# Kernel optimization log

Measured on AMD Instinct MI355X. Metric: run time of the kernel, lower is better.

The kernel has to match this reference:

```python
import jax, jax.numpy as jnp
import numpy as np

EMB = 768
B, LD, LW, LH = 2, 8, 8, 8        # LR grid = number of windows per axis
HD, HW, HH = 32, 32, 32           # HR volume
LN_EPS = 1e-5


def setup_inputs() -> dict:
    key = jax.random.key(0)
    ks = jax.random.split(key, 12)
    s = 1.0 / np.sqrt(EMB)
    inp = {
        "LR_image": jax.random.normal(ks[0], (B, LD, LW, LH, EMB), jnp.float32),
        "HR_image": jax.random.normal(ks[1], (B, HD, HW, HH, EMB), jnp.float32),
        "Wq_w": jax.random.uniform(ks[2], (EMB, EMB), jnp.float32, -s, s),
        "Wq_b": jax.random.uniform(ks[3], (EMB,), jnp.float32, -s, s),
        "Wk_w": jax.random.uniform(ks[4], (EMB, EMB), jnp.float32, -s, s),
        "Wk_b": jax.random.uniform(ks[5], (EMB,), jnp.float32, -s, s),
        "Wv_w": jax.random.uniform(ks[6], (EMB, EMB), jnp.float32, -s, s),
        "Wv_b": jax.random.uniform(ks[7], (EMB,), jnp.float32, -s, s),
        "Wo_w": jax.random.uniform(ks[8], (EMB, EMB), jnp.float32, -s, s),
        "Wo_b": jax.random.uniform(ks[9], (EMB,), jnp.float32, -s, s),
        "ln_g": jnp.ones((EMB,), jnp.float32),
        "ln_b": jnp.zeros((EMB,), jnp.float32),
        "S_d": 4, "S_w": 4, "S_h": 4,
    }
    return inp


def _window_partition(x, S_d, S_w, S_h):
    # x: [B, D, W, H, C] -> [B, N_blocks, S_d*S_w*S_h, C]
    b, d, w, h, c = x.shape
    x = x.reshape(b, d // S_d, S_d, w // S_w, S_w, h // S_h, S_h, c)
    x = jnp.transpose(x, (0, 2, 4, 6, 1, 3, 5, 7))  # [B,Sd,Sw,Sh,Db,Wb,Hb,C]
    x = x.reshape(b, S_d * S_w * S_h, -1, c)
    return jnp.transpose(x, (0, 2, 1, 3))  # [B, N_blocks, S, C]


def reference(LR_image, HR_image, Wq_w, Wq_b, Wk_w, Wk_b, Wv_w, Wv_b,
              Wo_w, Wo_b, ln_g, ln_b, S_d, S_w, S_h):
    b = LR_image.shape[0]
    c = LR_image.shape[-1]
    # queries: [B, N, 1, C]
    q_in = LR_image.reshape(b, -1, c)[:, :, None, :]
    # windowed keys/values: [B, N, S, C]
    hr = _window_partition(HR_image, S_d, S_w, S_h)
    q = q_in @ Wq_w.T + Wq_b
    k = hr @ Wk_w.T + Wk_b
    v = hr @ Wv_w.T + Wv_b
    scale = 1.0 / jnp.sqrt(jnp.asarray(c, q.dtype))
    scores = jnp.einsum('bnqc,bnsc->bnqs', q, k) * scale  # [B,N,1,S]
    attn = jax.nn.softmax(scores, axis=-1)
    x = jnp.einsum('bnqs,bnsc->bnqc', attn, v).reshape(b, -1, c)
    x = x @ Wo_w.T + Wo_b
    res = q.reshape(b, -1, c) + x  # residual with projected queries
    mu = jnp.mean(res, axis=-1, keepdims=True)
    var = jnp.var(res, axis=-1, keepdims=True)
    return (res - mu) / jnp.sqrt(var + LN_EPS) * ln_g + ln_b
```

## Files before the change

### kernel.cpp

```cpp
#include <hip/hip_runtime.h>
#include <hip/hip_bf16.h>
#include <math.h>

#define EMB 768
#define NB 2
#define NWIN 512
#define NROWS (NB*NWIN)
#define SWIN 64
#define HRDIM 32
#define ROWF (NROWS*EMB)
#define WELEM (EMB*EMB)

using bfrag = __attribute__((ext_vector_type(8))) short;
using f32x4 = __attribute__((ext_vector_type(4))) float;

#define GL16(g, l)  __builtin_amdgcn_global_load_lds(                         \
    (const __attribute__((address_space(1))) void*)(g),                       \
    (__attribute__((address_space(3))) void*)(l), 16, 0, 0)

__global__ __launch_bounds__(256)
void prep_kernel(const float* __restrict__ LR, __hip_bfloat16* __restrict__ LRb,
                 const float* __restrict__ Wq, __hip_bfloat16* __restrict__ Wqb,
                 const float* __restrict__ Wo, __hip_bfloat16* __restrict__ Wob,
                 __hip_bfloat16* __restrict__ WqTb,
                 const float* __restrict__ Wk, __hip_bfloat16* __restrict__ WkTb,
                 const float* __restrict__ Wv, __hip_bfloat16* __restrict__ WvTb,
                 const float* __restrict__ bq, const float* __restrict__ bv,
                 const float* __restrict__ bo,
                 float* __restrict__ bqk, float* __restrict__ bvo) {
  __shared__ float tile[32][33];
  const int bx = blockIdx.x;
  const int t = threadIdx.x;

  if (bx < 960) {
    const float* in; __hip_bfloat16* out; int i;
    if (bx < 384)      { in = LR; out = LRb; i = bx * 256 + t; }
    else if (bx < 672) { in = Wq; out = Wqb; i = (bx - 384) * 256 + t; }
    else               { in = Wo; out = Wob; i = (bx - 672) * 256 + t; }
    float4 a = *(const float4*)&in[(size_t)i * 8];
    float4 b = *(const float4*)&in[(size_t)i * 8 + 4];
    __hip_bfloat16 o[8];
    o[0] = __float2bfloat16(a.x); o[1] = __float2bfloat16(a.y);
    o[2] = __float2bfloat16(a.z); o[3] = __float2bfloat16(a.w);
    o[4] = __float2bfloat16(b.x); o[5] = __float2bfloat16(b.y);
    o[6] = __float2bfloat16(b.z); o[7] = __float2bfloat16(b.w);
    *(uint4*)&out[(size_t)i * 8] = *(const uint4*)o;
  } else if (bx < 2688) {
    int idx = bx - 960;
    int z = idx / 576, rem = idx % 576;
    int bi = rem % 24, bj = rem / 24;
    const float* in; __hip_bfloat16* out;
    if (z == 0)      { in = Wq; out = WqTb; }
    else if (z == 1) { in = Wk; out = WkTb; }
    else             { in = Wv; out = WvTb; }
    const int c = t & 31, r8 = t >> 5;
#pragma unroll
    for (int rr = 0; rr < 4; ++rr) {
      int r = r8 + rr * 8;
      tile[c][r] = in[(size_t)(bi * 32 + r) * EMB + bj * 32 + c];
    }
    __syncthreads();
#pragma unroll
    for (int rr = 0; rr < 4; ++rr) {
      int n = r8 + rr * 8;
      out[(size_t)(bj * 32 + n) * EMB + bi * 32 + c] = __float2bfloat16(tile[n][c]);
    }
  } else {
    int idx = bx - 2688;
    if (idx < 12) {
      __shared__ float red[4][64];
      const int io = t & 63, cg = t >> 6;
      const int i = idx * 64 + io;
      float s = 0.f;
#pragma unroll 8
      for (int c = cg; c < EMB; c += 4)
        s = fmaf(bq[c], Wk[(size_t)c * EMB + i], s);
      red[cg][io] = s;
      __syncthreads();
      if (cg == 0)
        bqk[i] = red[0][io] + red[1][io] + red[2][io] + red[3][io];
    } else {
      const int w = t >> 6, lane = t & 63;
      const int p = (idx - 12) * 4 + w;
      float s = 0.f;
#pragma unroll
      for (int r = 0; r < 12; ++r) {
        int n = lane + r * 64;
        s = fmaf(Wo[(size_t)p * EMB + n], bv[n], s);
      }
#pragma unroll
      for (int o = 32; o > 0; o >>= 1) s += __shfl_xor(s, o, 64);
      if (lane == 0) bvo[p] = bo[p] + s;
    }
  }
}

template<bool BIAS, bool WF32, bool WB16, bool RESID>
__global__ __launch_bounds__(256)
void gemm128(const __hip_bfloat16* __restrict__ A0,
             const __hip_bfloat16* __restrict__ A1,
             const __hip_bfloat16* __restrict__ B0,
             const __hip_bfloat16* __restrict__ B1,
             const float* __restrict__ bias0, const float* __restrict__ bias1,
             float* __restrict__ Cf0, float* __restrict__ Cf1,
             __hip_bfloat16* __restrict__ Cb0, __hip_bfloat16* __restrict__ Cb1,
             const float* __restrict__ R0, const float* __restrict__ R1,
             int N) {
  constexpr int K = EMB;
  constexpr int NT = K / 64;
  const int zi = blockIdx.z;
  const __hip_bfloat16* A  = zi ? A1 : A0;
  const __hip_bfloat16* Bm = zi ? B1 : B0;
  const float* bias = zi ? bias1 : bias0;
  float* Cf = zi ? Cf1 : Cf0;
  __hip_bfloat16* Cb = zi ? Cb1 : Cb0;
  const float* R = zi ? R1 : R0;

  __shared__ short lsA[3][128 * 64];
  __shared__ short lsB[3][128 * 64];
  const int t = threadIdx.x;
  const int w = t >> 6, lane = t & 63;
  const int lr = lane & 15, lk = lane >> 4;
  const int wr = w >> 1, wc = w & 1;
  const int m0 = blockIdx.y * 128, n0 = blockIdx.x * 128;

  const int r0 = t >> 3;
  const int kc = (t & 7) ^ (r0 & 7);
  const __hip_bfloat16* aptr = A + (size_t)(m0 + r0) * K + kc * 8;
  const __hip_bfloat16* bptr = Bm + (size_t)(n0 + r0) * K + kc * 8;
  const int wb512 = w * 512;

#define STAGE128(sl, ko)                                                      \
  do {                                                                        \
    GL16(aptr + 0 * 32 * K + (ko), &lsA[sl][0 * 2048 + wb512]);               \
    GL16(aptr + 1 * 32 * K + (ko), &lsA[sl][1 * 2048 + wb512]);               \
    GL16(aptr + 2 * 32 * K + (ko), &lsA[sl][2 * 2048 + wb512]);               \
    GL16(aptr + 3 * 32 * K + (ko), &lsA[sl][3 * 2048 + wb512]);               \
    GL16(bptr + 0 * 32 * K + (ko), &lsB[sl][0 * 2048 + wb512]);               \
    GL16(bptr + 1 * 32 * K + (ko), &lsB[sl][1 * 2048 + wb512]);               \
    GL16(bptr + 2 * 32 * K + (ko), &lsB[sl][2 * 2048 + wb512]);               \
    GL16(bptr + 3 * 32 * K + (ko), &lsB[sl][3 * 2048 + wb512]);               \
  } while (0)

  int aoff[4][2], boff[4][2];
#pragma unroll
  for (int f = 0; f < 4; ++f) {
    int ar = wr * 64 + f * 16 + lr;
    int br = wc * 64 + f * 16 + lr;
#pragma unroll
    for (int ks = 0; ks < 2; ++ks) {
      aoff[f][ks] = ar * 64 + ((((ks << 2) | lk) ^ (ar & 7)) << 3);
      boff[f][ks] = br * 64 + ((((ks << 2) | lk) ^ (br & 7)) << 3);
    }
  }

  f32x4 acc[4][4];
#pragma unroll
  for (int i = 0; i < 4; ++i)
#pragma unroll
    for (int j = 0; j < 4; ++j) acc[i][j] = (f32x4){0.f, 0.f, 0.f, 0.f};

  STAGE128(0, 0);
  STAGE128(1, 64);

#pragma unroll
  for (int kt = 0; kt < NT; ++kt) {
    if (kt + 2 < NT) {
      constexpr int s3[NT + 2] = {0,1,2,0,1,2,0,1,2,0,1,2,0,1};
      STAGE128(s3[kt + 2], (kt + 2) * 64);
    }
    if (kt + 2 < NT)      asm volatile("s_waitcnt vmcnt(16)" ::: "memory");
    else if (kt + 1 < NT) asm volatile("s_waitcnt vmcnt(8)" ::: "memory");
    else                  asm volatile("s_waitcnt vmcnt(0)" ::: "memory");
    __builtin_amdgcn_sched_barrier(0);
    __builtin_amdgcn_s_barrier();

    const int cur = kt % 3;
#pragma unroll
    for (int ks = 0; ks < 2; ++ks) {
      bfrag a_[4], b_[4];
#pragma unroll
      for (int f = 0; f < 4; ++f) {
        a_[f] = *(const bfrag*)&lsA[cur][aoff[f][ks]];
        b_[f] = *(const bfrag*)&lsB[cur][boff[f][ks]];
      }
#pragma unroll
      for (int i = 0; i < 4; ++i)
#pragma unroll
        for (int j = 0; j < 4; ++j)
          acc[i][j] = __builtin_amdgcn_mfma_f32_16x16x32_bf16(
              a_[i], b_[j], acc[i][j], 0, 0, 0);
    }

    asm volatile("s_waitcnt lgkmcnt(0)" ::: "memory");
    __builtin_amdgcn_s_barrier();
    __builtin_amdgcn_sched_barrier(0);
  }
#undef STAGE128

  float bs[4];
#pragma unroll
  for (int j = 0; j < 4; ++j)
    bs[j] = BIAS ? bias[n0 + wc * 64 + j * 16 + lr] : 0.f;

#pragma unroll
  for (int i = 0; i < 4; ++i) {
#pragma unroll
    for (int j = 0; j < 4; ++j) {
      int n = n0 + wc * 64 + j * 16 + lr;
#pragma unroll
      for (int q = 0; q < 4; ++q) {
        int m = m0 + wr * 64 + i * 16 + lk * 4 + q;
        float v = acc[i][j][q] + bs[j];
        if (RESID) v += R[(size_t)m * N + n];
        if (WF32) Cf[(size_t)m * N + n] = v;
        if (WB16) Cb[(size_t)m * N + n] = __float2bfloat16(v);
      }
    }
  }
}

__global__ __launch_bounds__(512)
void attn_kernel(const float* __restrict__ HR, const float* __restrict__ qt,
                 __hip_bfloat16* __restrict__ zb) {
  const int g = blockIdx.x;
  const int b = g >> 9;
  const int n = g & 511;
  const int db = n >> 6, wb = (n >> 3) & 7, hb = n & 7;

  __shared__ float zp[8][EMB];
  __shared__ float ml[8][2];

  const int t = threadIdx.x;
  const int w = t >> 6, lane = t & 63;

  float4 qv[3];
#pragma unroll
  for (int r = 0; r < 3; ++r)
    qv[r] = *(const float4*)&qt[(size_t)g * EMB + (lane + r * 64) * 4];

  const float* rows[8];
#pragma unroll
  for (int i = 0; i < 8; ++i) {
    int s = w * 8 + i;
    int D = db * 4 + (s >> 4), W = wb * 4 + ((s >> 2) & 3), H = hb * 4 + (s & 3);
    rows[i] = HR + (size_t)((((b * HRDIM + D) * HRDIM + W) * HRDIM + H)) * EMB;
  }

  const float scale = 0.036084391824351615f;
  float m = -3.0e38f, l = 0.f;
  float4 z0 = {0,0,0,0}, z1 = {0,0,0,0}, z2 = {0,0,0,0};

  float4 h0 = *(const float4*)&rows[0][lane * 4];
  float4 h1 = *(const float4*)&rows[0][(lane + 64) * 4];
  float4 h2 = *(const float4*)&rows[0][(lane + 128) * 4];

#pragma unroll
  for (int i = 0; i < 8; ++i) {
    float4 n0, n1, n2;
    if (i < 7) {
      n0 = *(const float4*)&rows[i + 1][lane * 4];
      n1 = *(const float4*)&rows[i + 1][(lane + 64) * 4];
      n2 = *(const float4*)&rows[i + 1][(lane + 128) * 4];
    }
    float p = 0.f;
    p = fmaf(h0.x, qv[0].x, p); p = fmaf(h0.y, qv[0].y, p);
    p = fmaf(h0.z, qv[0].z, p); p = fmaf(h0.w, qv[0].w, p);
    p = fmaf(h1.x, qv[1].x, p); p = fmaf(h1.y, qv[1].y, p);
    p = fmaf(h1.z, qv[1].z, p); p = fmaf(h1.w, qv[1].w, p);
    p = fmaf(h2.x, qv[2].x, p); p = fmaf(h2.y, qv[2].y, p);
    p = fmaf(h2.z, qv[2].z, p); p = fmaf(h2.w, qv[2].w, p);
#pragma unroll
    for (int o = 32; o > 0; o >>= 1) p += __shfl_xor(p, o, 64);
    p *= scale;
    float mn = fmaxf(m, p);
    float f = expf(m - mn);
    float e = expf(p - mn);
    z0.x = fmaf(e, h0.x, z0.x * f); z0.y = fmaf(e, h0.y, z0.y * f);
    z0.z = fmaf(e, h0.z, z0.z * f); z0.w = fmaf(e, h0.w, z0.w * f);
    z1.x = fmaf(e, h1.x, z1.x * f); z1.y = fmaf(e, h1.y, z1.y * f);
    z1.z = fmaf(e, h1.z, z1.z * f); z1.w = fmaf(e, h1.w, z1.w * f);
    z2.x = fmaf(e, h2.x, z2.x * f); z2.y = fmaf(e, h2.y, z2.y * f);
    z2.z = fmaf(e, h2.z, z2.z * f); z2.w = fmaf(e, h2.w, z2.w * f);
    l = fmaf(l, f, e);
    m = mn;
    if (i < 7) { h0 = n0; h1 = n1; h2 = n2; }
  }

  *(float4*)&zp[w][lane * 4] = z0;
  *(float4*)&zp[w][(lane + 64) * 4] = z1;
  *(float4*)&zp[w][(lane + 128) * 4] = z2;
  if (lane == 0) { ml[w][0] = m; ml[w][1] = l; }
  __syncthreads();

  if (t < 384) {
    float M = -3.0e38f;
#pragma unroll
    for (int w8 = 0; w8 < 8; ++w8) M = fmaxf(M, ml[w8][0]);
    float L = 0.f, a0 = 0.f, a1 = 0.f;
#pragma unroll
    for (int w8 = 0; w8 < 8; ++w8) {
      float ew = expf(ml[w8][0] - M);
      L = fmaf(ml[w8][1], ew, L);
      float2 v = *(const float2*)&zp[w8][t * 2];
      a0 = fmaf(v.x, ew, a0);
      a1 = fmaf(v.y, ew, a1);
    }
    float rl = 1.f / L;
    __hip_bfloat16 o[2];
    o[0] = __float2bfloat16(a0 * rl);
    o[1] = __float2bfloat16(a1 * rl);
    *(unsigned*)&zb[(size_t)g * EMB + t * 2] = *(const unsigned*)o;
  }
}

__global__ __launch_bounds__(256)
void ln_kernel(const float* __restrict__ R, const float* __restrict__ gma,
               const float* __restrict__ bta, float* __restrict__ out) {
  const int row = blockIdx.x;
  const int t = threadIdx.x;
  const int wave = t >> 6, lane = t & 63;
  __shared__ float red[4];

  float v[3];
  float s = 0.f;
#pragma unroll
  for (int r = 0; r < 3; ++r) {
    int c = t + r * 256;
    v[r] = R[(size_t)row * EMB + c];
    s += v[r];
  }
#pragma unroll
  for (int o = 32; o > 0; o >>= 1) s += __shfl_xor(s, o, 64);
  if (lane == 0) red[wave] = s;
  __syncthreads();
  float mu = (red[0] + red[1] + red[2] + red[3]) * (1.f / EMB);
  __syncthreads();

  float q = 0.f;
#pragma unroll
  for (int r = 0; r < 3; ++r) {
    float d = v[r] - mu;
    q += d * d;
  }
#pragma unroll
  for (int o = 32; o > 0; o >>= 1) q += __shfl_xor(q, o, 64);
  if (lane == 0) red[wave] = q;
  __syncthreads();
  float var = (red[0] + red[1] + red[2] + red[3]) * (1.f / EMB);
  float inv = rsqrtf(var + 1e-5f);

#pragma unroll
  for (int r = 0; r < 3; ++r) {
    int c = t + r * 256;
    out[(size_t)row * EMB + c] = (v[r] - mu) * inv * gma[c] + bta[c];
  }
}

extern "C" void kernel_launch(void* const* d_in, const int* in_sizes, int n_in,
                              void* d_out, int out_size, void* d_ws, size_t ws_size,
                              hipStream_t stream) {
  const float* LR  = (const float*)d_in[0];
  const float* HR  = (const float*)d_in[1];
  const float* Wq  = (const float*)d_in[2];
  const float* bq  = (const float*)d_in[3];
  const float* Wk  = (const float*)d_in[4];
  const float* Wv  = (const float*)d_in[6];
  const float* bv  = (const float*)d_in[7];
  const float* Wo  = (const float*)d_in[8];
  const float* bo  = (const float*)d_in[9];
  const float* lng = (const float*)d_in[10];
  const float* lnb = (const float*)d_in[11];
  float* out = (float*)d_out;

  char* ws = (char*)d_ws;
  float* Qf = (float*)(ws + 0);
  float* qt = (float*)(ws + 3145728);
  float* x  = (float*)(ws + 6291456);
  __hip_bfloat16* LRb  = (__hip_bfloat16*)(ws +  9437184);
  __hip_bfloat16* zb   = (__hip_bfloat16*)(ws + 11010048);
  __hip_bfloat16* Wqb  = (__hip_bfloat16*)(ws + 12582912);
  __hip_bfloat16* Wob  = (__hip_bfloat16*)(ws + 13762560);
  __hip_bfloat16* WqTb = (__hip_bfloat16*)(ws + 14942208);
  __hip_bfloat16* WkTb = (__hip_bfloat16*)(ws + 16121856);
  __hip_bfloat16* WvTb = (__hip_bfloat16*)(ws + 17301504);
  __hip_bfloat16* Wqkb = (__hip_bfloat16*)(ws + 18481152);
  __hip_bfloat16* Wvob = (__hip_bfloat16*)(ws + 19660800);
  float* bqk = (float*)(ws + 20840448);
  float* bvo = (float*)(ws + 20843520);

  dim3 blk(256);

  prep_kernel<<<dim3(2892), blk, 0, stream>>>(
      LR, LRb, Wq, Wqb, Wo, Wob, WqTb, Wk, WkTb, Wv, WvTb,
      bq, bv, bo, bqk, bvo);
  gemm128<false, false, true, false><<<dim3(6, 6, 2), blk, 0, stream>>>(
      WkTb, Wob, WqTb, WvTb, nullptr, nullptr,
      nullptr, nullptr, Wqkb, Wvob, nullptr, nullptr, EMB);
  gemm128<true, true, false, false><<<dim3(6, 8, 2), blk, 0, stream>>>(
      LRb, LRb, Wqb, Wqkb, bq, bqk, Qf, qt, nullptr, nullptr,
      nullptr, nullptr, EMB);
  attn_kernel<<<dim3(NROWS), dim3(512), 0, stream>>>(HR, qt, zb);
  gemm128<true, true, false, true><<<dim3(6, 8, 1), blk, 0, stream>>>(
      zb, zb, Wvob, Wvob, bvo, bvo, x, x, nullptr, nullptr, Qf, Qf, EMB);
  ln_kernel<<<dim3(NROWS), blk, 0, stream>>>(x, lng, lnb, out);
}
```

Before: 87.52 us.

## Compute qt from projected Q instead of folded Wq·Wk; merge GEMMs with atomic dependency

Drops the precomputed Wq^T·Wk weight product and the bq·Wk bias. The key-folded query qt is now computed as Q_bf16 @ Wk, which picks up the query bias implicitly, so one weight-weight GEMM and the WqT transpose go away. The Q projection, the Wv·Wo fold and the qt GEMM are merged into a single three-slice launch. The qt slice spin-waits on a global atomic counter that the 48 Q tiles increment, which removes kernel launches. The risks are deadlock if the z=2 blocks are scheduled before the z=0 blocks and fill the GPU (bounded by an iteration cap), and the GEMM templates becoming runtime branches.

```diff
diff --git a/kernel.cpp b/kernel.cpp
--- a/kernel.cpp
+++ b/kernel.cpp
@@ -22,12 +22,10 @@
 void prep_kernel(const float* __restrict__ LR, __hip_bfloat16* __restrict__ LRb,
                  const float* __restrict__ Wq, __hip_bfloat16* __restrict__ Wqb,
                  const float* __restrict__ Wo, __hip_bfloat16* __restrict__ Wob,
-                 __hip_bfloat16* __restrict__ WqTb,
                  const float* __restrict__ Wk, __hip_bfloat16* __restrict__ WkTb,
                  const float* __restrict__ Wv, __hip_bfloat16* __restrict__ WvTb,
-                 const float* __restrict__ bq, const float* __restrict__ bv,
-                 const float* __restrict__ bo,
-                 float* __restrict__ bqk, float* __restrict__ bvo) {
+                 const float* __restrict__ bv, const float* __restrict__ bo,
+                 float* __restrict__ bvo, int* __restrict__ ctr) {
   __shared__ float tile[32][33];
   const int bx = blockIdx.x;
   const int t = threadIdx.x;
@@ -45,14 +43,13 @@
     o[4] = __float2bfloat16(b.x); o[5] = __float2bfloat16(b.y);
     o[6] = __float2bfloat16(b.z); o[7] = __float2bfloat16(b.w);
     *(uint4*)&out[(size_t)i * 8] = *(const uint4*)o;
-  } else if (bx < 2688) {
+  } else if (bx < 2112) {
     int idx = bx - 960;
     int z = idx / 576, rem = idx % 576;
     int bi = rem % 24, bj = rem / 24;
     const float* in; __hip_bfloat16* out;
-    if (z == 0)      { in = Wq; out = WqTb; }
-    else if (z == 1) { in = Wk; out = WkTb; }
-    else             { in = Wv; out = WvTb; }
+    if (z == 0) { in = Wk; out = WkTb; }
+    else        { in = Wv; out = WvTb; }
     const int c = t & 31, r8 = t >> 5;
 #pragma unroll
     for (int rr = 0; rr < 4; ++rr) {
@@ -66,55 +63,60 @@
       out[(size_t)(bj * 32 + n) * EMB + bi * 32 + c] = __float2bfloat16(tile[n][c]);
     }
   } else {
-    int idx = bx - 2688;
-    if (idx < 12) {
-      __shared__ float red[4][64];
-      const int io = t & 63, cg = t >> 6;
-      const int i = idx * 64 + io;
-      float s = 0.f;
-#pragma unroll 8
-      for (int c = cg; c < EMB; c += 4)
-        s = fmaf(bq[c], Wk[(size_t)c * EMB + i], s);
-      red[cg][io] = s;
-      __syncthreads();
-      if (cg == 0)
-        bqk[i] = red[0][io] + red[1][io] + red[2][io] + red[3][io];
-    } else {
-      const int w = t >> 6, lane = t & 63;
-      const int p = (idx - 12) * 4 + w;
-      float s = 0.f;
-#pragma unroll
-      for (int r = 0; r < 12; ++r) {
-        int n = lane + r * 64;
-        s = fmaf(Wo[(size_t)p * EMB + n], bv[n], s);
-      }
-#pragma unroll
-      for (int o = 32; o > 0; o >>= 1) s += __shfl_xor(s, o, 64);
-      if (lane == 0) bvo[p] = bo[p] + s;
-    }
+    int idx = bx - 2112;
+    if (idx == 0 && t == 0) *ctr = 0;
+    const int w = t >> 6, lane = t & 63;
+    const int p = idx * 4 + w;
+    float s = 0.f;
+#pragma unroll
+    for (int r = 0; r < 12; ++r) {
+      int n = lane + r * 64;
+      s = fmaf(Wo[(size_t)p * EMB + n], bv[n], s);
+    }
+#pragma unroll
+    for (int o = 32; o > 0; o >>= 1) s += __shfl_xor(s, o, 64);
+    if (lane == 0) bvo[p] = bo[p] + s;
   }
 }
 
-template<bool BIAS, bool WF32, bool WB16, bool RESID>
 __global__ __launch_bounds__(256)
 void gemm128(const __hip_bfloat16* __restrict__ A0,
+             const __hip_bfloat16* __restrict__ B0,
+             const float* __restrict__ bias0, float* __restrict__ Cf0,
+             __hip_bfloat16* __restrict__ Cb0, const float* __restrict__ R0,
              const __hip_bfloat16* __restrict__ A1,
-             const __hip_bfloat16* __restrict__ B0,
              const __hip_bfloat16* __restrict__ B1,
-             const float* __restrict__ bias0, const float* __restrict__ bias1,
-             float* __restrict__ Cf0, float* __restrict__ Cf1,
-             __hip_bfloat16* __restrict__ Cb0, __hip_bfloat16* __restrict__ Cb1,
-             const float* __restrict__ R0, const float* __restrict__ R1,
-             int N) {
+             const float* __restrict__ bias1, float* __restrict__ Cf1,
+             __hip_bfloat16* __restrict__ Cb1,
+             const __hip_bfloat16* __restrict__ A2,
+             const __hip_bfloat16* __restrict__ B2,
+             const float* __restrict__ bias2, float* __restrict__ Cf2,
+             __hip_bfloat16* __restrict__ Cb2,
+             int* ctr, int N, int ylim1) {
   constexpr int K = EMB;
   constexpr int NT = K / 64;
   const int zi = blockIdx.z;
-  const __hip_bfloat16* A  = zi ? A1 : A0;
-  const __hip_bfloat16* Bm = zi ? B1 : B0;
-  const float* bias = zi ? bias1 : bias0;
-  float* Cf = zi ? Cf1 : Cf0;
-  __hip_bfloat16* Cb = zi ? Cb1 : Cb0;
-  const float* R = zi ? R1 : R0;
+  const __hip_bfloat16* A  = (zi == 0) ? A0 : (zi == 1) ? A1 : A2;
+  const __hip_bfloat16* Bm = (zi == 0) ? B0 : (zi == 1) ? B1 : B2;
+  const float* bias = (zi == 0) ? bias0 : (zi == 1) ? bias1 : bias2;
+  float* Cf = (zi == 0) ? Cf0 : (zi == 1) ? Cf1 : Cf2;
+  __hip_bfloat16* Cb = (zi == 0) ? Cb0 : (zi == 1) ? Cb1 : Cb2;
+  const float* R = (zi == 0) ? R0 : nullptr;
+
+  if (zi == 1 && (int)blockIdx.y >= ylim1) return;
+
+  if (ctr && zi == 2) {
+    if ((threadIdx.x & 63) == 0) {
+      int it = 0;
+      while (__hip_atomic_load(ctr, __ATOMIC_ACQUIRE,
+                               __HIP_MEMORY_SCOPE_AGENT) < 48 &&
+             it < (1 << 20)) {
+        __builtin_amdgcn_s_sleep(4);
+        ++it;
+      }
+    }
+    __syncthreads();
+  }
 
   __shared__ short lsA[3][128 * 64];
   __shared__ short lsB[3][128 * 64];
@@ -201,7 +203,7 @@
   float bs[4];
 #pragma unroll
   for (int j = 0; j < 4; ++j)
-    bs[j] = BIAS ? bias[n0 + wc * 64 + j * 16 + lr] : 0.f;
+    bs[j] = bias ? bias[n0 + wc * 64 + j * 16 + lr] : 0.f;
 
 #pragma unroll
   for (int i = 0; i < 4; ++i) {
@@ -212,11 +214,19 @@
       for (int q = 0; q < 4; ++q) {
         int m = m0 + wr * 64 + i * 16 + lk * 4 + q;
         float v = acc[i][j][q] + bs[j];
-        if (RESID) v += R[(size_t)m * N + n];
-        if (WF32) Cf[(size_t)m * N + n] = v;
-        if (WB16) Cb[(size_t)m * N + n] = __float2bfloat16(v);
+        if (R) v += R[(size_t)m * N + n];
+        if (Cf) Cf[(size_t)m * N + n] = v;
+        if (Cb) Cb[(size_t)m * N + n] = __float2bfloat16(v);
       }
     }
+  }
+
+  if (ctr && zi == 0) {
+    __threadfence();
+    __syncthreads();
+    if (threadIdx.x == 0)
+      __hip_atomic_fetch_add(ctr, 1, __ATOMIC_RELEASE,
+                             __HIP_MEMORY_SCOPE_AGENT);
   }
 }
 
@@ -379,29 +389,33 @@
   float* x  = (float*)(ws + 6291456);
   __hip_bfloat16* LRb  = (__hip_bfloat16*)(ws +  9437184);
   __hip_bfloat16* zb   = (__hip_bfloat16*)(ws + 11010048);
-  __hip_bfloat16* Wqb  = (__hip_bfloat16*)(ws + 12582912);
-  __hip_bfloat16* Wob  = (__hip_bfloat16*)(ws + 13762560);
-  __hip_bfloat16* WqTb = (__hip_bfloat16*)(ws + 14942208);
-  __hip_bfloat16* WkTb = (__hip_bfloat16*)(ws + 16121856);
-  __hip_bfloat16* WvTb = (__hip_bfloat16*)(ws + 17301504);
-  __hip_bfloat16* Wqkb = (__hip_bfloat16*)(ws + 18481152);
-  __hip_bfloat16* Wvob = (__hip_bfloat16*)(ws + 19660800);
-  float* bqk = (float*)(ws + 20840448);
-  float* bvo = (float*)(ws + 20843520);
+  __hip_bfloat16* Qbb  = (__hip_bfloat16*)(ws + 12582912);
+  __hip_bfloat16* Wqb  = (__hip_bfloat16*)(ws + 14155776);
+  __hip_bfloat16* WkTb = (__hip_bfloat16*)(ws + 15335424);
+  __hip_bfloat16* WvTb = (__hip_bfloat16*)(ws + 16515072);
+  __hip_bfloat16* Wob  = (__hip_bfloat16*)(ws + 17694720);
+  __hip_bfloat16* Wvob = (__hip_bfloat16*)(ws + 18874368);
+  float* bvo = (float*)(ws + 20054016);
+  int*   ctr = (int*)(ws + 20971520);
 
   dim3 blk(256);
 
-  prep_kernel<<<dim3(2892), blk, 0, stream>>>(
-      LR, LRb, Wq, Wqb, Wo, Wob, WqTb, Wk, WkTb, Wv, WvTb,
-      bq, bv, bo, bqk, bvo);
-  gemm128<false, false, true, false><<<dim3(6, 6, 2), blk, 0, stream>>>(
-      WkTb, Wob, WqTb, WvTb, nullptr, nullptr,
-      nullptr, nullptr, Wqkb, Wvob, nullptr, nullptr, EMB);
-  gemm128<true, true, false, false><<<dim3(6, 8, 2), blk, 0, stream>>>(
-      LRb, LRb, Wqb, Wqkb, bq, bqk, Qf, qt, nullptr, nullptr,
-      nullptr, nullptr, EMB);
+  prep_kernel<<<dim3(2304), blk, 0, stream>>>(
+      LR, LRb, Wq, Wqb, Wo, Wob, Wk, WkTb, Wv, WvTb, bv, bo, bvo, ctr);
+
+  gemm128<<<dim3(6, 8, 3), blk, 0, stream>>>(
+      LRb, Wqb, bq, Qf, Qbb, nullptr,
+      Wob, WvTb, nullptr, nullptr, Wvob,
+      Qbb, WkTb, nullptr, qt, nullptr,
+      ctr, EMB, 6);
+
   attn_kernel<<<dim3(NROWS), dim3(512), 0, stream>>>(HR, qt, zb);
-  gemm128<true, true, false, true><<<dim3(6, 8, 1), blk, 0, stream>>>(
-      zb, zb, Wvob, Wvob, bvo, bvo, x, x, nullptr, nullptr, Qf, Qf, EMB);
+
+  gemm128<<<dim3(6, 8, 1), blk, 0, stream>>>(
+      zb, Wvob, bvo, x, nullptr, Qf,
+      nullptr, nullptr, nullptr, nullptr, nullptr,
+      nullptr, nullptr, nullptr, nullptr, nullptr,
+      nullptr, EMB, 6);
+
   ln_kernel<<<dim3(NROWS), blk, 0, stream>>>(x, lng, lnb, out);
 }
```

New measurement: 115.7 us. 1.32x slower.
